# Performance work log

Hardware: AMD Instinct MI355X
Metric: run time of the kernel (lower is better)

## Reference

```python
import jax, jax.numpy as jnp
import numpy as np

THRESHOLD = 0.625  # module default; is_positive=True path


def setup_inputs() -> dict:
    key = jax.random.key(0)
    k1, k2 = jax.random.split(key)
    x = jax.random.normal(k1, (16, 512, 64, 64), dtype=jnp.float32)  # [B,C,H,W]
    # trunc_normal_(std=0.02) init for the dictionary parameter [N, C]
    negative_dict = 0.02 * jax.random.truncated_normal(k2, -2.0, 2.0, (512, 512), dtype=jnp.float32)
    return {"x": x, "negative_dict": negative_dict}


def reference(x, negative_dict):
    # Normalize along channel dim (dim=1 for feature, dim=1 for [N,C] dict)
    f_norm = x / jnp.linalg.norm(x, axis=1, keepdims=True)
    d_norm = negative_dict / jnp.linalg.norm(negative_dict, axis=1, keepdims=True)
    # cosine similarity: [B,C,H,W] x [N,C] -> [B,N,H,W]
    sim = jnp.einsum('bchw,nc->bnhw', f_norm, d_norm)
    dist = (1.0 - sim) * 0.5  # anomalous probability per dict element
    apm = jnp.min(dist, axis=1, keepdims=True)      # [B,1,H,W]
    index = jnp.argmin(dist, axis=1)                # [B,H,W]
    # high_pass: replace features whose apm < threshold by nearest dict element
    replace_map = (apm < THRESHOLD).astype(x.dtype)  # [B,1,H,W]
    restructured = negative_dict[index]              # [B,H,W,C] gather
    restructured = jnp.transpose(restructured, (0, 3, 1, 2))  # [B,C,H,W]
    out = x * (1.0 - replace_map) + restructured * replace_map
    return out
```

## Files before the change

### kernel.cpp

```cpp
#include <hip/hip_runtime.h>
#include <math.h>

#define C_DIM  512
#define N_DICT 512
#define HW     4096

typedef _Float16 h8_t __attribute__((ext_vector_type(8)));
typedef _Float16 h4_t __attribute__((ext_vector_type(4)));
typedef float    f4_t __attribute__((ext_vector_type(4)));

#define SCALE_D 16384.0f
#define SCALE_X 256.0f

__global__ __launch_bounds__(64) void dict_prep(const float* __restrict__ dict,
                                                _Float16* __restrict__ d1p,
                                                _Float16* __restrict__ d2p,
                                                float* __restrict__ invn) {
    const int n  = blockIdx.x;
    const int kq = threadIdx.x;
    const float* __restrict__ row = dict + n * C_DIM;
    const float4* rp = (const float4*)(row + kq * 8);
    float4 va = rp[0], vb = rp[1];
    float vv[8] = {va.x, va.y, va.z, va.w, vb.x, vb.y, vb.z, vb.w};
    float s = 0.f;
    h8_t h1, h2;
#pragma unroll
    for (int j = 0; j < 8; ++j) {
        float v = vv[j];
        s = fmaf(v, v, s);
        float xs = v * SCALE_D;
        _Float16 a = (_Float16)xs;
        float r = xs - (float)a;
        h1[j] = a;
        h2[j] = (_Float16)r;
    }
    const size_t dest = ((size_t)(n >> 4) * 64 + kq) * 16 + (n & 15);
    *(h8_t*)(d1p + dest * 8) = h1;
    *(h8_t*)(d2p + dest * 8) = h2;
#pragma unroll
    for (int off = 32; off > 0; off >>= 1) s += __shfl_down(s, off, 64);
    if (kq == 0) invn[n] = (1.0f / sqrtf(s)) * (1.0f / (SCALE_D * SCALE_X));
}

__global__ __launch_bounds__(512, 4) void negdict_mfma2(
        const float* __restrict__ x,
        const float* __restrict__ dict,
        const _Float16* __restrict__ d1p,
        const _Float16* __restrict__ d2p,
        const float* __restrict__ invn,
        float* __restrict__ out) {
    __shared__ __attribute__((aligned(16))) unsigned char lds_x[2][32 * 272];
    __shared__ float ls_best[8][32];
    __shared__ int   ls_idx[8][32];
    __shared__ float ls_ssq[8][64];
    __shared__ int   fin[32];

    const int pg   = blockIdx.x;
    const int b    = pg >> 7;
    const int pix0 = (pg & 127) << 5;
    const int t    = (int)threadIdx.x;
    const int lane = t & 63;
    const int w    = __builtin_amdgcn_readfirstlane(t >> 6);

    const float* __restrict__ xb = x + (size_t)b * (C_DIM * HW);

    const int spix = lane & 31;
    const int kql  = (w & 3) * 2 + (lane >> 5);
    const int hf   = w >> 2;
    const int choff = kql * 8 + hf * 4;
    const int wr_hi = spix * 272 + kql * 32 + hf * 8;
    const int wr_lo = wr_hi + 16;

    const int arow = lane & 15;
    const int akq  = lane >> 4;
    const _Float16* __restrict__ a1w = d1p + (size_t)w * 32768 + lane * 8;
    const _Float16* __restrict__ a2w = d2p + (size_t)w * 32768 + lane * 8;

    const int rbase_b = (lane & 15) * 272 + akq * 32;

    f4_t acc[4][2];
#pragma unroll
    for (int rf = 0; rf < 4; ++rf)
#pragma unroll
        for (int cf = 0; cf < 2; ++cf)
            acc[rf][cf] = (f4_t){0.f, 0.f, 0.f, 0.f};

    float sumsq = 0.f;

    {
        const float* xp = xb + (size_t)choff * HW + pix0 + spix;
        float xvv[4] = {xp[0], xp[HW], xp[2 * HW], xp[3 * HW]};
        h4_t p1, p2;
#pragma unroll
        for (int i = 0; i < 4; ++i) {
            float v = xvv[i];
            sumsq = fmaf(v, v, sumsq);
            float xs = v * SCALE_X;
            _Float16 a = (_Float16)xs;
            float r = xs - (float)a;
            p1[i] = a;
            p2[i] = (_Float16)r;
        }
        *(h4_t*)(&lds_x[0][wr_hi]) = p1;
        *(h4_t*)(&lds_x[0][wr_lo]) = p2;
    }
    __syncthreads();

    int cur = 0;
#pragma unroll 1
    for (int step = 0; step < 8; ++step) {
        float nxt0 = 0.f, nxt1 = 0.f, nxt2 = 0.f, nxt3 = 0.f;
        if (step < 7) {
            const float* xp = xb + (size_t)(step * 64 + 64 + choff) * HW + pix0 + spix;
            nxt0 = xp[0]; nxt1 = xp[HW]; nxt2 = xp[2 * HW]; nxt3 = xp[3 * HW];
        }

        const unsigned char* lb = lds_x[cur];
#pragma unroll
        for (int ks = 0; ks < 2; ++ks) {
            h8_t A1[4], A2[4];
#pragma unroll
            for (int rf = 0; rf < 4; ++rf) {
                const int eo = rf * 8192 + step * 1024 + ks * 512;
                A1[rf] = *(const h8_t*)(a1w + eo);
                A2[rf] = *(const h8_t*)(a2w + eo);
            }
            h8_t B1[2], B2[2];
#pragma unroll
            for (int cf = 0; cf < 2; ++cf) {
                B1[cf] = *(const h8_t*)(lb + rbase_b + cf * 4352 + ks * 128);
                B2[cf] = *(const h8_t*)(lb + rbase_b + cf * 4352 + ks * 128 + 16);
            }
#pragma unroll
            for (int rf = 0; rf < 4; ++rf) {
#pragma unroll
                for (int cf = 0; cf < 2; ++cf) {
                    acc[rf][cf] = __builtin_amdgcn_mfma_f32_16x16x32_f16(A1[rf], B1[cf], acc[rf][cf], 0, 0, 0);
                    acc[rf][cf] = __builtin_amdgcn_mfma_f32_16x16x32_f16(A1[rf], B2[cf], acc[rf][cf], 0, 0, 0);
                    acc[rf][cf] = __builtin_amdgcn_mfma_f32_16x16x32_f16(A2[rf], B1[cf], acc[rf][cf], 0, 0, 0);
                }
            }
        }

        if (step < 7) {
            unsigned char* lw = lds_x[cur ^ 1];
            float xvv[4] = {nxt0, nxt1, nxt2, nxt3};
            h4_t p1, p2;
#pragma unroll
            for (int i = 0; i < 4; ++i) {
                float v = xvv[i];
                sumsq = fmaf(v, v, sumsq);
                float xs = v * SCALE_X;
                _Float16 a = (_Float16)xs;
                float r = xs - (float)a;
                p1[i] = a;
                p2[i] = (_Float16)r;
            }
            *(h4_t*)(lw + wr_hi) = p1;
            *(h4_t*)(lw + wr_lo) = p2;
        }
        __syncthreads();
        cur ^= 1;
    }

    float best0 = -3.0e38f, best1 = -3.0e38f;
    int bi0 = 0, bi1 = 0;
    const int rbase = w * 64 + akq * 4;
#pragma unroll
    for (int rf = 0; rf < 4; ++rf) {
#pragma unroll
        for (int i = 0; i < 4; ++i) {
            const int row = rbase + rf * 16 + i;
            const float inv = invn[row];
            float v0 = acc[rf][0][i] * inv;
            float v1 = acc[rf][1][i] * inv;
            if (v0 > best0 || (v0 == best0 && row < bi0)) { best0 = v0; bi0 = row; }
            if (v1 > best1 || (v1 == best1 && row < bi1)) { best1 = v1; bi1 = row; }
        }
    }
#pragma unroll
    for (int off = 16; off <= 32; off <<= 1) {
        float o0 = __shfl_xor(best0, off, 64); int m0 = __shfl_xor(bi0, off, 64);
        float o1 = __shfl_xor(best1, off, 64); int m1 = __shfl_xor(bi1, off, 64);
        if (o0 > best0 || (o0 == best0 && m0 < bi0)) { best0 = o0; bi0 = m0; }
        if (o1 > best1 || (o1 == best1 && m1 < bi1)) { best1 = o1; bi1 = m1; }
    }
    if (akq == 0) {
        ls_best[w][ 0 + arow] = best0; ls_idx[w][ 0 + arow] = bi0;
        ls_best[w][16 + arow] = best1; ls_idx[w][16 + arow] = bi1;
    }
    ls_ssq[w][lane] = sumsq;
    __syncthreads();

    if (t < 32) {
        const int p = t;
        float fb = ls_best[0][p]; int fi = ls_idx[0][p];
#pragma unroll
        for (int q = 1; q < 8; ++q) {
            float v = ls_best[q][p]; int id = ls_idx[q][p];
            if (v > fb || (v == fb && id < fi)) { fb = v; fi = id; }
        }
        float ss = 0.f;
#pragma unroll
        for (int q = 0; q < 8; ++q) ss += ls_ssq[q][p] + ls_ssq[q][p + 32];
        fin[p] = (fb > (-0.25f * sqrtf(ss))) ? fi : -1;
    }
    __syncthreads();

    const int fi = fin[lane & 31];
    const bool rep = fi >= 0;
    const unsigned long long need_x = __ballot(!rep);
    const float* __restrict__ drow = dict + (size_t)(rep ? fi : 0) * C_DIM;
    const int gpix = pix0 + (lane & 31);
    float* __restrict__ ob = out + (size_t)b * (C_DIM * HW) + gpix;
    const int c0 = w * 64 + (lane >> 5) * 2;
#pragma unroll 4
    for (int i = 0; i < 16; ++i) {
        const int c = c0 + i * 4;
        float2 v = *(const float2*)(drow + c);
        if (need_x) {
            if (!rep) {
                v.x = xb[(size_t)c * HW + gpix];
                v.y = xb[(size_t)(c + 1) * HW + gpix];
            }
        }
        ob[(size_t)c * HW]       = v.x;
        ob[(size_t)(c + 1) * HW] = v.y;
    }
}

__global__ __launch_bounds__(64) void dict_inv_norm(const float* __restrict__ dict,
                                                    float* __restrict__ inv_norm) {
    const int n = blockIdx.x;
    const int lane = threadIdx.x;
    const float* row = dict + n * C_DIM;
    float s = 0.f;
#pragma unroll
    for (int j = 0; j < C_DIM / 64; ++j) {
        float v = row[j * 64 + lane];
        s = fmaf(v, v, s);
    }
#pragma unroll
    for (int off = 32; off > 0; off >>= 1)
        s += __shfl_down(s, off, 64);
    if (lane == 0) inv_norm[n] = 1.0f / sqrtf(s);
}

#define ACCS(F) F(0) F(1) F(2) F(3) F(4) F(5) F(6) F(7) \
                F(8) F(9) F(10) F(11) F(12) F(13) F(14) F(15) \
                F(16) F(17) F(18) F(19) F(20) F(21) F(22) F(23) \
                F(24) F(25) F(26) F(27) F(28) F(29) F(30) F(31)

#define DECL_ACC(i) float acc##i = 0.f;

#define ROW_FMA(i) { const float* __restrict__ dr = dbase + (size_t)(i) * C_DIM; \
    acc##i = fmaf(dr[0], xk0, acc##i); \
    acc##i = fmaf(dr[1], xk1, acc##i); \
    acc##i = fmaf(dr[2], xk2, acc##i); \
    acc##i = fmaf(dr[3], xk3, acc##i); \
    acc##i = fmaf(dr[4], xk4, acc##i); \
    acc##i = fmaf(dr[5], xk5, acc##i); \
    acc##i = fmaf(dr[6], xk6, acc##i); \
    acc##i = fmaf(dr[7], xk7, acc##i); }

#define ARGMAX(i) { float s = acc##i * invn[i]; \
    if (s > best) { best = s; bestn = n0 + (i); } }

__global__ __launch_bounds__(1024, 4) void negdict_main(const float* __restrict__ x,
                                                        const float* __restrict__ dict,
                                                        const float* __restrict__ inv_norm,
                                                        float* __restrict__ out) {
    const int pg   = blockIdx.x;
    const int b    = pg >> 6;
    const int pix0 = (pg & 63) << 6;
    const int lane = (int)(threadIdx.x & 63);
    const int wv   = __builtin_amdgcn_readfirstlane((int)(threadIdx.x >> 6));
    const int pix  = pix0 + lane;
    const int n0   = wv * 32;

    const float* __restrict__ xb = x + (size_t)b * C_DIM * HW;

    ACCS(DECL_ACC)
    float sumsq = 0.f;

    for (int kc = 0; kc < C_DIM; kc += 8) {
        const float* __restrict__ xp = xb + (size_t)kc * HW + pix;
        float xk0 = xp[0 * HW];
        float xk1 = xp[1 * HW];
        float xk2 = xp[2 * HW];
        float xk3 = xp[3 * HW];
        float xk4 = xp[4 * HW];
        float xk5 = xp[5 * HW];
        float xk6 = xp[6 * HW];
        float xk7 = xp[7 * HW];
        sumsq = fmaf(xk0, xk0, sumsq);
        sumsq = fmaf(xk1, xk1, sumsq);
        sumsq = fmaf(xk2, xk2, sumsq);
        sumsq = fmaf(xk3, xk3, sumsq);
        sumsq = fmaf(xk4, xk4, sumsq);
        sumsq = fmaf(xk5, xk5, sumsq);
        sumsq = fmaf(xk6, xk6, sumsq);
        sumsq = fmaf(xk7, xk7, sumsq);

        const float* __restrict__ dbase = dict + (size_t)n0 * C_DIM + kc;
        ACCS(ROW_FMA)
    }

    const float* __restrict__ invn = inv_norm + n0;
    float best = -3.0e38f;
    int   bestn = n0;
    ACCS(ARGMAX)

    __shared__ float ls_best[16][64];
    __shared__ int   ls_idx[16][64];
    ls_best[wv][lane] = best;
    ls_idx[wv][lane]  = bestn;
    __syncthreads();

    float fbest = ls_best[0][lane];
    int   fidx  = ls_idx[0][lane];
#pragma unroll
    for (int q = 1; q < 16; ++q) {
        float v  = ls_best[q][lane];
        int   id = ls_idx[q][lane];
        if (v > fbest) { fbest = v; fidx = id; }
    }

    const bool replace = fbest > (-0.25f * sqrtf(sumsq));
    const unsigned long long need_x = __ballot(!replace);

    float* __restrict__ ob = out + (size_t)b * C_DIM * HW;
    const float* __restrict__ drow = dict + (size_t)fidx * C_DIM;

    const int c0 = wv * 32;
#pragma unroll 8
    for (int c = c0; c < c0 + 32; ++c) {
        float v = drow[c];
        if (need_x) {
            float xv = xb[(size_t)c * HW + pix];
            if (!replace) v = xv;
        }
        ob[(size_t)c * HW + pix] = v;
    }
}

extern "C" void kernel_launch(void* const* d_in, const int* in_sizes, int n_in,
                              void* d_out, int out_size, void* d_ws, size_t ws_size,
                              hipStream_t stream) {
    const float* x    = (const float*)d_in[0];
    const float* dict = (const float*)d_in[1];
    float* out        = (float*)d_out;

    const size_t need = (size_t)N_DICT * C_DIM * 2 * sizeof(_Float16) + N_DICT * sizeof(float);
    if (ws_size >= need) {
        _Float16* d1p = (_Float16*)d_ws;
        _Float16* d2p = d1p + (size_t)N_DICT * C_DIM;
        float* invn   = (float*)(d2p + (size_t)N_DICT * C_DIM);
        dict_prep<<<N_DICT, 64, 0, stream>>>(dict, d1p, d2p, invn);
        negdict_mfma2<<<2048, 512, 0, stream>>>(x, dict, d1p, d2p, invn, out);
    } else {
        float* inv_norm = (float*)d_ws;
        dict_inv_norm<<<N_DICT, 64, 0, stream>>>(dict, inv_norm);
        negdict_main<<<1024, 1024, 0, stream>>>(x, dict, inv_norm, out);
    }
}
```

Measured before the change: 369.4 us.

## Double K-step size to 128 channels per stage and raise occupancy hint

The x tile staged in LDS now covers 128 channels per pipeline stage instead of 64, so the main loop runs 4 iterations with 4 k-substeps each instead of 8 with 2. That halves the barriers and prefetch rounds, and each thread now loads 8 channels with full 8-wide fp16 LDS writes. The launch bound hint rises from 4 to 6 waves per SIMD. The cost is more LDS (about 34KB per block for x), which may cap blocks per CU, and more prefetch registers in flight, which the tighter occupancy hint may force to spill.

```diff
diff --git a/kernel.cpp b/kernel.cpp
--- a/kernel.cpp
+++ b/kernel.cpp
@@ -42,14 +42,14 @@
     if (kq == 0) invn[n] = (1.0f / sqrtf(s)) * (1.0f / (SCALE_D * SCALE_X));
 }
 
-__global__ __launch_bounds__(512, 4) void negdict_mfma2(
+__global__ __launch_bounds__(512, 6) void negdict_mfma3(
         const float* __restrict__ x,
         const float* __restrict__ dict,
         const _Float16* __restrict__ d1p,
         const _Float16* __restrict__ d2p,
         const float* __restrict__ invn,
         float* __restrict__ out) {
-    __shared__ __attribute__((aligned(16))) unsigned char lds_x[2][32 * 272];
+    __shared__ __attribute__((aligned(16))) unsigned char lds_x[2][32 * 528];
     __shared__ float ls_best[8][32];
     __shared__ int   ls_idx[8][32];
     __shared__ float ls_ssq[8][64];
@@ -64,19 +64,17 @@
 
     const float* __restrict__ xb = x + (size_t)b * (C_DIM * HW);
 
-    const int spix = lane & 31;
-    const int kql  = (w & 3) * 2 + (lane >> 5);
-    const int hf   = w >> 2;
-    const int choff = kql * 8 + hf * 4;
-    const int wr_hi = spix * 272 + kql * 32 + hf * 8;
-    const int wr_lo = wr_hi + 16;
+    const int spix  = lane & 31;
+    const int octl  = w * 2 + (lane >> 5);
+    const int choff = octl * 8;
+    const int wr    = spix * 528 + octl * 32;
 
     const int arow = lane & 15;
     const int akq  = lane >> 4;
     const _Float16* __restrict__ a1w = d1p + (size_t)w * 32768 + lane * 8;
     const _Float16* __restrict__ a2w = d2p + (size_t)w * 32768 + lane * 8;
 
-    const int rbase_b = (lane & 15) * 272 + akq * 32;
+    const int rb = arow * 528 + akq * 32;
 
     f4_t acc[4][2];
 #pragma unroll
@@ -89,47 +87,50 @@
 
     {
         const float* xp = xb + (size_t)choff * HW + pix0 + spix;
-        float xvv[4] = {xp[0], xp[HW], xp[2 * HW], xp[3 * HW]};
-        h4_t p1, p2;
-#pragma unroll
-        for (int i = 0; i < 4; ++i) {
-            float v = xvv[i];
+        h8_t p1, p2;
+#pragma unroll
+        for (int j = 0; j < 8; ++j) {
+            float v = xp[(size_t)j * HW];
             sumsq = fmaf(v, v, sumsq);
             float xs = v * SCALE_X;
             _Float16 a = (_Float16)xs;
             float r = xs - (float)a;
-            p1[i] = a;
-            p2[i] = (_Float16)r;
-        }
-        *(h4_t*)(&lds_x[0][wr_hi]) = p1;
-        *(h4_t*)(&lds_x[0][wr_lo]) = p2;
+            p1[j] = a;
+            p2[j] = (_Float16)r;
+        }
+        *(h8_t*)(&lds_x[0][wr])      = p1;
+        *(h8_t*)(&lds_x[0][wr + 16]) = p2;
     }
     __syncthreads();
 
     int cur = 0;
 #pragma unroll 1
-    for (int step = 0; step < 8; ++step) {
-        float nxt0 = 0.f, nxt1 = 0.f, nxt2 = 0.f, nxt3 = 0.f;
-        if (step < 7) {
-            const float* xp = xb + (size_t)(step * 64 + 64 + choff) * HW + pix0 + spix;
-            nxt0 = xp[0]; nxt1 = xp[HW]; nxt2 = xp[2 * HW]; nxt3 = xp[3 * HW];
+    for (int step = 0; step < 4; ++step) {
+        float n0, n1, n2, n3, n4, n5, n6, n7;
+        if (step < 3) {
+            const float* xp = xb + (size_t)(step * 128 + 128 + choff) * HW + pix0 + spix;
+            n0 = xp[0];              n1 = xp[(size_t)1 * HW];
+            n2 = xp[(size_t)2 * HW]; n3 = xp[(size_t)3 * HW];
+            n4 = xp[(size_t)4 * HW]; n5 = xp[(size_t)5 * HW];
+            n6 = xp[(size_t)6 * HW]; n7 = xp[(size_t)7 * HW];
         }
 
         const unsigned char* lb = lds_x[cur];
 #pragma unroll
-        for (int ks = 0; ks < 2; ++ks) {
+        for (int ks = 0; ks < 4; ++ks) {
+            const int ksg = step * 4 + ks;
             h8_t A1[4], A2[4];
 #pragma unroll
             for (int rf = 0; rf < 4; ++rf) {
-                const int eo = rf * 8192 + step * 1024 + ks * 512;
+                const int eo = rf * 8192 + ksg * 512;
                 A1[rf] = *(const h8_t*)(a1w + eo);
                 A2[rf] = *(const h8_t*)(a2w + eo);
             }
             h8_t B1[2], B2[2];
 #pragma unroll
             for (int cf = 0; cf < 2; ++cf) {
-                B1[cf] = *(const h8_t*)(lb + rbase_b + cf * 4352 + ks * 128);
-                B2[cf] = *(const h8_t*)(lb + rbase_b + cf * 4352 + ks * 128 + 16);
+                B1[cf] = *(const h8_t*)(lb + rb + cf * 8448 + ks * 128);
+                B2[cf] = *(const h8_t*)(lb + rb + cf * 8448 + ks * 128 + 16);
             }
 #pragma unroll
             for (int rf = 0; rf < 4; ++rf) {
@@ -142,22 +143,22 @@
             }
         }
 
-        if (step < 7) {
+        if (step < 3) {
             unsigned char* lw = lds_x[cur ^ 1];
-            float xvv[4] = {nxt0, nxt1, nxt2, nxt3};
-            h4_t p1, p2;
-#pragma unroll
-            for (int i = 0; i < 4; ++i) {
-                float v = xvv[i];
+            float xvv[8] = {n0, n1, n2, n3, n4, n5, n6, n7};
+            h8_t p1, p2;
+#pragma unroll
+            for (int j = 0; j < 8; ++j) {
+                float v = xvv[j];
                 sumsq = fmaf(v, v, sumsq);
                 float xs = v * SCALE_X;
                 _Float16 a = (_Float16)xs;
                 float r = xs - (float)a;
-                p1[i] = a;
-                p2[i] = (_Float16)r;
-            }
-            *(h4_t*)(lw + wr_hi) = p1;
-            *(h4_t*)(lw + wr_lo) = p2;
+                p1[j] = a;
+                p2[j] = (_Float16)r;
+            }
+            *(h8_t*)(lw + wr)      = p1;
+            *(h8_t*)(lw + wr + 16) = p2;
         }
         __syncthreads();
         cur ^= 1;
@@ -357,7 +358,7 @@
         _Float16* d2p = d1p + (size_t)N_DICT * C_DIM;
         float* invn   = (float*)(d2p + (size_t)N_DICT * C_DIM);
         dict_prep<<<N_DICT, 64, 0, stream>>>(dict, d1p, d2p, invn);
-        negdict_mfma2<<<2048, 512, 0, stream>>>(x, dict, d1p, d2p, invn, out);
+        negdict_mfma3<<<2048, 512, 0, stream>>>(x, dict, d1p, d2p, invn, out);
     } else {
         float* inv_norm = (float*)d_ws;
         dict_inv_norm<<<N_DICT, 64, 0, stream>>>(dict, inv_norm);
```

New measurement: 425.9 us. +15.3%, slower.
